# Kernel tuning notes

Hardware: AMD Instinct MI355X
Metric: run time of the kernel (lower is better)

Reference implementation:

```python
import jax, jax.numpy as jnp
import numpy as np

B, N, DIM = 4, 4096, 1024
HEADS, DIM_HEAD, M = 16, 64, 128
DIM_INNER = HEADS * DIM_HEAD
SCALE = DIM_HEAD ** -0.5


def setup_inputs() -> dict:
    key = jax.random.key(0)
    ks = jax.random.split(key, 7)
    x = jax.random.normal(ks[0], (B, N, DIM), dtype=jnp.float32)
    mask = jax.random.bernoulli(ks[1], 0.9, (B, N))  # bool [b, n]
    W_qkv = jax.random.normal(ks[2], (DIM, 3 * DIM_INNER), dtype=jnp.float32) * (DIM ** -0.5)
    agent_tokens = jax.random.normal(ks[3], (HEADS, M, DIM_HEAD), dtype=jnp.float32) * 0.02
    W_qa = jax.random.normal(ks[4], (HEADS, HEADS), dtype=jnp.float32) * (HEADS ** -0.5)
    W_ak = jax.random.normal(ks[5], (HEADS, HEADS), dtype=jnp.float32) * (HEADS ** -0.5)
    W_out = jax.random.normal(ks[6], (DIM_INNER, DIM), dtype=jnp.float32) * (DIM_INNER ** -0.5)
    return {"x": x, "mask": mask, "W_qkv": W_qkv, "agent_tokens": agent_tokens,
            "W_qa": W_qa, "W_ak": W_ak, "W_out": W_out}


def reference(x, mask, W_qkv, agent_tokens, W_qa, W_ak, W_out):
    b, n, _ = x.shape
    h, m, d = agent_tokens.shape
    # qkv projection -> [3, b, h, n, d]  (layout matches 'b n (qkv h d)')
    qkv = (x @ W_qkv).reshape(b, n, 3, h, d).transpose(2, 0, 3, 1, 4)
    q, k, v = qkv[0], qkv[1], qkv[2]
    a = agent_tokens * SCALE  # [h, m, d]
    # stage 1: query-agent similarities [b, h, n, m]
    qa_sim = jnp.einsum('bhid,hjd->bhij', q, a)
    # stage 2: agent-key similarities [b, h, m, n]
    ak_sim = jnp.einsum('hid,bhjd->bhij', a, k)
    max_neg = -jnp.finfo(ak_sim.dtype).max
    ak_sim = jnp.where(mask[:, None, None, :], ak_sim, max_neg)
    qa_attn = jax.nn.softmax(qa_sim, axis=-1)
    ak_attn = jax.nn.softmax(ak_sim, axis=-1)
    # talking heads: 1x1 conv over head dim == head-mixing matmul
    qa_attn = jnp.einsum('gh,bhij->bgij', W_qa, qa_attn)
    ak_attn = jnp.einsum('gh,bhij->bgij', W_ak, ak_attn)
    agent_out = jnp.einsum('bhmn,bhnd->bhmd', ak_attn, v)    # [b, h, m, d]
    out = jnp.einsum('bhnm,bhmd->bhnd', qa_attn, agent_out)  # [b, h, n, d]
    out = jnp.where(mask[:, None, :, None], out, 0.0)
    out = out.transpose(0, 2, 1, 3).reshape(b, n, h * d)
    return out @ W_out
```

## Files before the change

kernel.cpp:

```cpp
#include <hip/hip_runtime.h>
#include <stdint.h>

#define DEVI __device__ __forceinline__

typedef __bf16 bf16x8 __attribute__((ext_vector_type(8)));
typedef float  f32x4  __attribute__((ext_vector_type(4)));
typedef unsigned int u32x2 __attribute__((ext_vector_type(2)));


DEVI unsigned short f2bf(float f) {
  union { float f; unsigned int u; } c; c.f = f;
  return (unsigned short)((c.u + 0x7fffu + ((c.u >> 16) & 1u)) >> 16);
}
DEVI float bf2f(unsigned short s) {
  union { unsigned int u; float f; } c; c.u = ((unsigned int)s) << 16;
  return c.f;
}
DEVI u32x2 pack4(float a, float b, float c, float d) {
  u32x2 r;
  r.x = (unsigned)f2bf(a) | ((unsigned)f2bf(b) << 16);
  r.y = (unsigned)f2bf(c) | ((unsigned)f2bf(d) << 16);
  return r;
}
DEVI bf16x8 ldg8(const unsigned short* p) { return *(const bf16x8*)p; }

DEVI void g2l16(const void* g, void* l) {
  __builtin_amdgcn_global_load_lds(
      (const __attribute__((address_space(1))) unsigned int*)g,
      (__attribute__((address_space(3))) unsigned int*)l, 16, 0, 0);
}

#define MFMA16(acc, a, b) acc = __builtin_amdgcn_mfma_f32_16x16x32_bf16((a), (b), (acc), 0, 0, 0)

#define VMCNT8() asm volatile("s_waitcnt vmcnt(8)")
#define VMCNT4() asm volatile("s_waitcnt vmcnt(4)")
#define VMCNT0() asm volatile("s_waitcnt vmcnt(0)")
#define SBAR()   __builtin_amdgcn_s_barrier()
#define SCHEDB() __builtin_amdgcn_sched_barrier(0)

__global__ __launch_bounds__(256) void k_prep(
    const float* __restrict__ x, const float* __restrict__ Wqkv,
    const float* __restrict__ ag, const float* __restrict__ Wout,
    unsigned short* __restrict__ Xb, unsigned short* __restrict__ WqkvT,
    unsigned short* __restrict__ Ab, unsigned short* __restrict__ WoT,
    float* __restrict__ rowsum)
{
  __shared__ float ldsT[32][33];
  const int tid = threadIdx.x;
  int bx = blockIdx.x;
  if (bx < 16384) {
    size_t i4 = ((size_t)bx * 256 + tid) * 4;
    f32x4 v = *(const f32x4*)&x[i4];
    *(u32x2*)&Xb[i4] = pack4(v[0], v[1], v[2], v[3]);
    return;
  }
  bx -= 16384;
  if (bx < 3072) {
    int jt = bx % 96, kt = bx / 96;
    int r32 = tid >> 3, c4 = (tid & 7) * 4;
    f32x4 v = *(const f32x4*)&Wqkv[(size_t)(kt * 32 + r32) * 3072 + jt * 32 + c4];
#pragma unroll
    for (int i = 0; i < 4; i++) ldsT[r32][c4 + i] = v[i];
    __syncthreads();
    float o0 = ldsT[c4 + 0][r32], o1 = ldsT[c4 + 1][r32];
    float o2 = ldsT[c4 + 2][r32], o3 = ldsT[c4 + 3][r32];
    *(u32x2*)&WqkvT[(size_t)(jt * 32 + r32) * 1024 + kt * 32 + c4] = pack4(o0, o1, o2, o3);
    return;
  }
  bx -= 3072;
  if (bx < 128) {
    size_t i4 = ((size_t)bx * 256 + tid) * 4;
    f32x4 v = *(const f32x4*)&ag[i4];
    *(u32x2*)&Ab[i4] = pack4(v[0] * 0.125f, v[1] * 0.125f, v[2] * 0.125f, v[3] * 0.125f);
    return;
  }
  bx -= 128;
  if (bx < 1024) {
    int ct = bx % 32, dt = bx / 32;
    int r32 = tid >> 3, c4 = (tid & 7) * 4;
    f32x4 v = *(const f32x4*)&Wout[(size_t)(dt * 32 + r32) * 1024 + ct * 32 + c4];
#pragma unroll
    for (int i = 0; i < 4; i++) ldsT[r32][c4 + i] = v[i];
    __syncthreads();
    float o0 = ldsT[c4 + 0][r32], o1 = ldsT[c4 + 1][r32];
    float o2 = ldsT[c4 + 2][r32], o3 = ldsT[c4 + 3][r32];
    *(u32x2*)&WoT[(size_t)(ct * 32 + r32) * 1024 + dt * 32 + c4] = pack4(o0, o1, o2, o3);
    return;
  }
  bx -= 1024;
  {
    const f32x4 z = {0.f, 0.f, 0.f, 0.f};
    *(f32x4*)&rowsum[((size_t)bx * 256 + tid) * 4] = z;
  }
}

DEVI void gemm_core_256(const unsigned short* __restrict__ A,
                        const unsigned short* __restrict__ Bt,
                        int row0, int col0, int swap,
                        unsigned short (*lds)[16384], f32x4 acc[8][4])
{
  const int tid = threadIdx.x, lane = tid & 63, w = tid >> 6;
  const int q = lane >> 4, r = lane & 15;
  const int wm = w >> 2, wn = w & 3;
  const int loff = r * 32 + ((q ^ ((r >> 1) & 3)) << 3);
  const int wslot = w * 512;
  const int scol = ((tid & 3) ^ ((tid >> 3) & 3)) << 3;
  const int srow = tid >> 2;
  const unsigned short* gA0 = A + (size_t)(row0 + srow) * 1024 + scol;
  const unsigned short* gA1 = gA0 + (size_t)128 * 1024;
  const unsigned short* gB0 = Bt + (size_t)(col0 + srow) * 1024 + scol;
  const unsigned short* gB1 = gB0 + (size_t)128 * 1024;
  const int aoff = (swap ? 8192 : 0) + wm * 4096;
  const int boff = (swap ? 0 : 8192) + wn * 2048;

  const f32x4 z = {0.f, 0.f, 0.f, 0.f};
#pragma unroll
  for (int i = 0; i < 8; i++)
#pragma unroll
    for (int j = 0; j < 4; j++) acc[i][j] = z;

#pragma unroll
  for (int pt = 0; pt < 3; ++pt) {
    unsigned short* lr = &lds[pt][0] + wslot;
    g2l16(gA0 + pt * 32, lr);
    g2l16(gA1 + pt * 32, lr + 4096);
    g2l16(gB0 + pt * 32, lr + 8192);
    g2l16(gB1 + pt * 32, lr + 12288);
  }
  VMCNT8();
  SBAR();

  for (int t = 0; t < 32; ++t) {
    const unsigned short* rp = &lds[t & 3][0];
    const unsigned short* pA = rp + aoff + loff;
    const unsigned short* pB = rp + boff + loff;
    bf16x8 af[4], bv[4];
#pragma unroll
    for (int ct = 0; ct < 4; ct++) bv[ct] = *(const bf16x8*)(pB + ct * 512);
#pragma unroll
    for (int rt = 0; rt < 4; rt++) af[rt] = *(const bf16x8*)(pA + rt * 512);
    SCHEDB();
    SBAR();
    if (t < 29) {
      unsigned short* lr = &lds[(t + 3) & 3][0] + wslot;
      size_t ko = (size_t)(t + 3) * 32;
      g2l16(gA0 + ko, lr);
      g2l16(gA1 + ko, lr + 4096);
      g2l16(gB0 + ko, lr + 8192);
      g2l16(gB1 + ko, lr + 12288);
    }
    __builtin_amdgcn_s_setprio(1);
#pragma unroll
    for (int rt = 0; rt < 4; rt++)
#pragma unroll
      for (int ct = 0; ct < 4; ct++) MFMA16(acc[rt][ct], af[rt], bv[ct]);
    __builtin_amdgcn_s_setprio(0);
#pragma unroll
    for (int rt = 0; rt < 4; rt++) af[rt] = *(const bf16x8*)(pA + (rt + 4) * 512);
    SCHEDB();
    if (t < 29)       { VMCNT8(); }
    else if (t == 29) { VMCNT4(); }
    else if (t == 30) { VMCNT0(); }
    SBAR();
    __builtin_amdgcn_s_setprio(1);
#pragma unroll
    for (int rt = 0; rt < 4; rt++)
#pragma unroll
      for (int ct = 0; ct < 4; ct++) MFMA16(acc[rt + 4][ct], af[rt], bv[ct]);
    __builtin_amdgcn_s_setprio(0);
  }
}

__global__ __launch_bounds__(512, 2) void k_gemm_qkv(
    const unsigned short* __restrict__ A, const unsigned short* __restrict__ Bt,
    unsigned short* __restrict__ Q, unsigned short* __restrict__ Kd,
    unsigned short* __restrict__ Vt)
{
  __shared__ __align__(16) unsigned short lds[4][16384];
  const int tid = threadIdx.x, lane = tid & 63, w = tid >> 6;
  const int q = lane >> 4, r = lane & 15, wm = w >> 2, wn = w & 3;
  const int row0 = blockIdx.x * 256, col0 = blockIdx.y * 256;
  const bool qk = blockIdx.y < 8;

  f32x4 acc[8][4];
  gemm_core_256(A, Bt, row0, col0, qk ? 1 : 0, lds, acc);

  const int b = row0 >> 12, row0b = row0 & 4095;
  if (qk) {
    unsigned short* dst = (col0 < 1024) ? Q : Kd;
    const int jb = (col0 & 1023) + wm * 128;
#pragma unroll
    for (int rt = 0; rt < 8; rt++)
#pragma unroll
      for (int ct = 0; ct < 4; ct++) {
        int j = jb + rt * 16 + 4 * q;
        int h = j >> 6, d0 = j & 63;
        int n = row0b + wn * 64 + ct * 16 + r;
        u32x2 pk = pack4(acc[rt][ct][0], acc[rt][ct][1], acc[rt][ct][2], acc[rt][ct][3]);
        *(u32x2*)&dst[(((size_t)(b * 16 + h)) * 4096 + n) * 64 + d0] = pk;
      }
  } else {
    const int jb = (col0 - 2048) + wn * 64;
#pragma unroll
    for (int rt = 0; rt < 8; rt++)
#pragma unroll
      for (int ct = 0; ct < 4; ct++) {
        int j = jb + ct * 16 + r;
        int h = j >> 6, d = j & 63;
        int n = row0b + wm * 128 + rt * 16 + 4 * q;
        u32x2 pk = pack4(acc[rt][ct][0], acc[rt][ct][1], acc[rt][ct][2], acc[rt][ct][3]);
        *(u32x2*)&Vt[(((size_t)(b * 16 + h)) * 64 + d) * 4096 + n] = pk;
      }
  }
}

__global__ __launch_bounds__(256, 2) void k_qk(
    const unsigned short* __restrict__ Q, const unsigned short* __restrict__ Kd,
    const unsigned short* __restrict__ Ab, const int* __restrict__ mask,
    unsigned short* __restrict__ QA, unsigned short* __restrict__ E,
    float* __restrict__ rowsum)
{
  const int tid = threadIdx.x, lane = tid & 63, w = tid >> 6;
  const int q = lane >> 4, r = lane & 15, wr = w >> 1, wc = w & 1;
  const int nt = blockIdx.x, h = blockIdx.y, b = blockIdx.z;
  const unsigned short* Qb = Q + (((size_t)(b * 16 + h)) * 4096 + nt * 128) * 64;
  const unsigned short* Kb = Kd + (((size_t)(b * 16 + h)) * 4096 + nt * 128) * 64;
  const unsigned short* Ah = Ab + (size_t)h * 8192;
  __shared__ float rs[2][128];
  const f32x4 z = {0.f, 0.f, 0.f, 0.f};

  {
    f32x4 acc[4][4];
#pragma unroll
    for (int i = 0; i < 4; i++)
#pragma unroll
      for (int j = 0; j < 4; j++) acc[i][j] = z;
#pragma unroll
    for (int ks = 0; ks < 2; ks++) {
      bf16x8 af[4], bv[4];
#pragma unroll
      for (int rt = 0; rt < 4; rt++) af[rt] = ldg8(Ah + (size_t)(64 * wr + 16 * rt + r) * 64 + ks * 32 + q * 8);
#pragma unroll
      for (int ct = 0; ct < 4; ct++) bv[ct] = ldg8(Qb + (size_t)(64 * wc + 16 * ct + r) * 64 + ks * 32 + q * 8);
#pragma unroll
      for (int rt = 0; rt < 4; rt++)
#pragma unroll
        for (int ct = 0; ct < 4; ct++) MFMA16(acc[rt][ct], af[rt], bv[ct]);
    }
    float cs[4];
#pragma unroll
    for (int ct = 0; ct < 4; ct++) {
      float s = 0.f;
#pragma unroll
      for (int rt = 0; rt < 4; rt++)
#pragma unroll
        for (int reg = 0; reg < 4; reg++) {
          float e = __expf(acc[rt][ct][reg]);
          acc[rt][ct][reg] = e; s += e;
        }
      s += __shfl_xor(s, 16); s += __shfl_xor(s, 32);
      cs[ct] = s;
    }
    if (q == 0) {
#pragma unroll
      for (int ct = 0; ct < 4; ct++) rs[wr][64 * wc + 16 * ct + r] = cs[ct];
    }
    __syncthreads();
#pragma unroll
    for (int ct = 0; ct < 4; ct++) {
      int nl = 64 * wc + 16 * ct + r;
      float inv = 1.0f / (rs[0][nl] + rs[1][nl]);
      int n = nt * 128 + nl;
      size_t base = (((size_t)(b * 16 + h)) * 4096 + n) * 128;
#pragma unroll
      for (int rt = 0; rt < 4; rt++) {
        int m0 = 64 * wr + 16 * rt + 4 * q;
        u32x2 pk = pack4(acc[rt][ct][0] * inv, acc[rt][ct][1] * inv,
                         acc[rt][ct][2] * inv, acc[rt][ct][3] * inv);
        *(u32x2*)&QA[base + m0] = pk;
      }
    }
  }
  __syncthreads();

  {
    f32x4 acc[4][4];
#pragma unroll
    for (int i = 0; i < 4; i++)
#pragma unroll
      for (int j = 0; j < 4; j++) acc[i][j] = z;
#pragma unroll
    for (int ks = 0; ks < 2; ks++) {
      bf16x8 af[4], bv[4];
#pragma unroll
      for (int rt = 0; rt < 4; rt++) af[rt] = ldg8(Kb + (size_t)(64 * wr + 16 * rt + r) * 64 + ks * 32 + q * 8);
#pragma unroll
      for (int ct = 0; ct < 4; ct++) bv[ct] = ldg8(Ah + (size_t)(64 * wc + 16 * ct + r) * 64 + ks * 32 + q * 8);
#pragma unroll
      for (int rt = 0; rt < 4; rt++)
#pragma unroll
        for (int ct = 0; ct < 4; ct++) MFMA16(acc[rt][ct], af[rt], bv[ct]);
    }
    float cs[4] = {0.f, 0.f, 0.f, 0.f};
#pragma unroll
    for (int rt = 0; rt < 4; rt++) {
      const int4 mkv = *(const int4*)&mask[b * 4096 + nt * 128 + 64 * wr + 16 * rt + 4 * q];
      int mka[4] = {mkv.x, mkv.y, mkv.z, mkv.w};
#pragma unroll
      for (int ct = 0; ct < 4; ct++) {
#pragma unroll
        for (int reg = 0; reg < 4; reg++) {
          float e = mka[reg] ? __expf(acc[rt][ct][reg]) : 0.0f;
          acc[rt][ct][reg] = e; cs[ct] += e;
        }
      }
    }
#pragma unroll
    for (int ct = 0; ct < 4; ct++) {
      float s = cs[ct];
      s += __shfl_xor(s, 16); s += __shfl_xor(s, 32);
      cs[ct] = s;
    }
    if (q == 0) {
#pragma unroll
      for (int ct = 0; ct < 4; ct++) rs[wr][64 * wc + 16 * ct + r] = cs[ct];
    }
#pragma unroll
    for (int ct = 0; ct < 4; ct++) {
      int m = 64 * wc + 16 * ct + r;
      size_t base = (((size_t)(b * 16 + h)) * 128 + m) * 4096;
#pragma unroll
      for (int rt = 0; rt < 4; rt++) {
        int n0 = nt * 128 + 64 * wr + 16 * rt + 4 * q;
        u32x2 pk = pack4(acc[rt][ct][0], acc[rt][ct][1], acc[rt][ct][2], acc[rt][ct][3]);
        *(u32x2*)&E[base + n0] = pk;
      }
    }
    __syncthreads();
    if (tid < 128) atomicAdd(&rowsum[(b * 16 + h) * 128 + tid], rs[0][tid] + rs[1][tid]);
  }
}

__global__ __launch_bounds__(256) void k_mix(
    const unsigned short* __restrict__ E, const float* __restrict__ rowsum,
    const float* __restrict__ Wak, unsigned short* __restrict__ MIX)
{
  const int tid = threadIdx.x;
  const int m = blockIdx.y, b = blockIdx.z;
  __shared__ float wv[256];
  __shared__ float inv[16];
  wv[tid] = Wak[tid];
  if (tid < 16) inv[tid] = 1.0f / rowsum[(b * 16 + tid) * 128 + m];
  __syncthreads();
  const int n0 = (blockIdx.x * 256 + tid) * 4;
  float p[16][4];
#pragma unroll
  for (int h = 0; h < 16; h++) {
    u32x2 v = *(const u32x2*)&E[(((size_t)(b * 16 + h)) * 128 + m) * 4096 + n0];
    float iv = inv[h];
    p[h][0] = bf2f((unsigned short)(v.x & 0xffff)) * iv;
    p[h][1] = bf2f((unsigned short)(v.x >> 16)) * iv;
    p[h][2] = bf2f((unsigned short)(v.y & 0xffff)) * iv;
    p[h][3] = bf2f((unsigned short)(v.y >> 16)) * iv;
  }
#pragma unroll
  for (int g = 0; g < 16; g++) {
    float s0 = 0.f, s1 = 0.f, s2 = 0.f, s3 = 0.f;
#pragma unroll
    for (int h = 0; h < 16; h++) {
      float wgh = wv[g * 16 + h];
      s0 += wgh * p[h][0]; s1 += wgh * p[h][1]; s2 += wgh * p[h][2]; s3 += wgh * p[h][3];
    }
    *(u32x2*)&MIX[(((size_t)(b * 16 + g)) * 128 + m) * 4096 + n0] = pack4(s0, s1, s2, s3);
  }
}

__global__ __launch_bounds__(256) void k_ao(
    const unsigned short* __restrict__ MIX, const unsigned short* __restrict__ Vt,
    float* __restrict__ P)
{
  const int tid = threadIdx.x, lane = tid & 63, w4 = tid >> 6;
  const int q = lane >> 4, r = lane & 15;
  const int kc = blockIdx.x, g = blockIdx.y, b = blockIdx.z;
  const unsigned short* Abase = MIX + ((size_t)(b * 16 + g)) * 128 * 4096;
  const unsigned short* Bbase = Vt + ((size_t)(b * 16 + g)) * 64 * 4096;
  f32x4 acc[2][4];
  const f32x4 z = {0.f, 0.f, 0.f, 0.f};
#pragma unroll
  for (int i = 0; i < 2; i++)
#pragma unroll
    for (int j = 0; j < 4; j++) acc[i][j] = z;
  for (int n = kc * 512; n < kc * 512 + 512; n += 32) {
    bf16x8 af[2], bv[4];
#pragma unroll
    for (int rt = 0; rt < 2; rt++) af[rt] = ldg8(Abase + (size_t)(32 * w4 + 16 * rt + r) * 4096 + n + q * 8);
#pragma unroll
    for (int ct = 0; ct < 4; ct++) bv[ct] = ldg8(Bbase + (size_t)(16 * ct + r) * 4096 + n + q * 8);
#pragma unroll
    for (int rt = 0; rt < 2; rt++)
#pragma unroll
      for (int ct = 0; ct < 4; ct++) MFMA16(acc[rt][ct], af[rt], bv[ct]);
  }
  float* Pp = P + (size_t)kc * 524288 + ((size_t)(b * 16 + g)) * 8192;
#pragma unroll
  for (int rt = 0; rt < 2; rt++)
#pragma unroll
    for (int ct = 0; ct < 4; ct++) {
      int m0 = 32 * w4 + 16 * rt + 4 * q, d = 16 * ct + r;
      *(f32x4*)&Pp[(size_t)d * 128 + m0] = acc[rt][ct];
    }
}

__global__ __launch_bounds__(256) void k_aored(
    const float* __restrict__ P, float* __restrict__ AOt)
{
  size_t i = ((size_t)blockIdx.x * 256 + threadIdx.x) * 4;
  f32x4 s = *(const f32x4*)&P[i];
#pragma unroll
  for (int kc = 1; kc < 8; kc++) {
    f32x4 v = *(const f32x4*)&P[(size_t)kc * 524288 + i];
    s[0] += v[0]; s[1] += v[1]; s[2] += v[2]; s[3] += v[3];
  }
  *(f32x4*)&AOt[i] = s;
}

__global__ __launch_bounds__(256) void k_mixqa(
    const unsigned short* __restrict__ QA, const float* __restrict__ Wqa,
    unsigned short* __restrict__ QAmix)
{
  const int tid = threadIdx.x;
  const int b = blockIdx.y;
  __shared__ float wv[256];
  wv[tid] = Wqa[tid];
  __syncthreads();
  const size_t i0 = ((size_t)blockIdx.x * 256 + tid) * 4;
  float p[16][4];
#pragma unroll
  for (int h = 0; h < 16; h++) {
    u32x2 v = *(const u32x2*)&QA[((size_t)(b * 16 + h)) * 524288 + i0];
    p[h][0] = bf2f((unsigned short)(v.x & 0xffff));
    p[h][1] = bf2f((unsigned short)(v.x >> 16));
    p[h][2] = bf2f((unsigned short)(v.y & 0xffff));
    p[h][3] = bf2f((unsigned short)(v.y >> 16));
  }
#pragma unroll
  for (int g = 0; g < 16; g++) {
    float s0 = 0.f, s1 = 0.f, s2 = 0.f, s3 = 0.f;
#pragma unroll
    for (int h = 0; h < 16; h++) {
      float wgh = wv[g * 16 + h];
      s0 += wgh * p[h][0]; s1 += wgh * p[h][1]; s2 += wgh * p[h][2]; s3 += wgh * p[h][3];
    }
    *(u32x2*)&QAmix[((size_t)(b * 16 + g)) * 524288 + i0] = pack4(s0, s1, s2, s3);
  }
}

__global__ __launch_bounds__(256) void k_o1(
    const unsigned short* __restrict__ QAmix, const float* __restrict__ AOt,
    unsigned short* __restrict__ out1)
{
  const int tid = threadIdx.x, lane = tid & 63, w4 = tid >> 6;
  const int q = lane >> 4, r = lane & 15;
  const int nt = blockIdx.x, g = blockIdx.y, b = blockIdx.z;
  const unsigned short* Bbase = QAmix + (((size_t)(b * 16 + g)) * 4096 + nt * 128) * 128;
  const float* Abase = AOt + ((size_t)(b * 16 + g)) * 8192;
  f32x4 acc[4][2];
  const f32x4 z = {0.f, 0.f, 0.f, 0.f};
#pragma unroll
  for (int i = 0; i < 4; i++)
#pragma unroll
    for (int j = 0; j < 2; j++) acc[i][j] = z;
#pragma unroll
  for (int ks = 0; ks < 4; ks++) {
    bf16x8 af[4], bv[2];
#pragma unroll
    for (int rt = 0; rt < 4; rt++) {
      const float* p = Abase + (size_t)(16 * rt + r) * 128 + ks * 32 + q * 8;
      f32x4 f0 = *(const f32x4*)p;
      f32x4 f1 = *(const f32x4*)(p + 4);
      bf16x8 t;
#pragma unroll
      for (int jj = 0; jj < 4; jj++) { t[jj] = (__bf16)f0[jj]; t[4 + jj] = (__bf16)f1[jj]; }
      af[rt] = t;
    }
#pragma unroll
    for (int ct = 0; ct < 2; ct++)
      bv[ct] = ldg8(Bbase + (size_t)(32 * w4 + 16 * ct + r) * 128 + ks * 32 + q * 8);
#pragma unroll
    for (int rt = 0; rt < 4; rt++)
#pragma unroll
      for (int ct = 0; ct < 2; ct++) MFMA16(acc[rt][ct], af[rt], bv[ct]);
  }
#pragma unroll
  for (int ct = 0; ct < 2; ct++) {
    int n = nt * 128 + 32 * w4 + 16 * ct + r;
    size_t base = ((size_t)b * 4096 + n) * 1024 + g * 64;
#pragma unroll
    for (int rt = 0; rt < 4; rt++) {
      int d0 = 16 * rt + 4 * q;
      u32x2 pk = pack4(acc[rt][ct][0], acc[rt][ct][1], acc[rt][ct][2], acc[rt][ct][3]);
      *(u32x2*)&out1[base + d0] = pk;
    }
  }
}

__global__ __launch_bounds__(512, 2) void k_fin2(
    const unsigned short* __restrict__ A, const unsigned short* __restrict__ Bt,
    const int* __restrict__ mask, float* __restrict__ out)
{
  __shared__ __align__(16) unsigned short lds[4][16384];
  const int tid = threadIdx.x, lane = tid & 63, w = tid >> 6;
  const int q = lane >> 4, r = lane & 15, wm = w >> 2, wn = w & 3;
  const int row0 = blockIdx.x * 256, col0 = blockIdx.y * 256;

  f32x4 acc[8][4];
  gemm_core_256(A, Bt, row0, col0, 0, lds, acc);

#pragma unroll
  for (int rt = 0; rt < 8; rt++) {
    const int4 mkv = *(const int4*)&mask[row0 + wm * 128 + rt * 16 + 4 * q];
    int mka[4] = {mkv.x, mkv.y, mkv.z, mkv.w};
#pragma unroll
    for (int reg = 0; reg < 4; reg++) {
      int row = row0 + wm * 128 + rt * 16 + 4 * q + reg;
#pragma unroll
      for (int ct = 0; ct < 4; ct++) {
        int c = col0 + wn * 64 + ct * 16 + r;
        out[(size_t)row * 1024 + c] = mka[reg] ? acc[rt][ct][reg] : 0.0f;
      }
    }
  }
}

extern "C" void kernel_launch(void* const* d_in, const int* in_sizes, int n_in,
                              void* d_out, int out_size, void* d_ws, size_t ws_size,
                              hipStream_t stream) {
  const float* x    = (const float*)d_in[0];
  const int*   mask = (const int*)d_in[1];
  const float* Wqkv = (const float*)d_in[2];
  const float* ag   = (const float*)d_in[3];
  const float* Wqa  = (const float*)d_in[4];
  const float* Wak  = (const float*)d_in[5];
  const float* Wout = (const float*)d_in[6];
  float* out = (float*)d_out;
  char* ws = (char*)d_ws;

  unsigned short* QA    = (unsigned short*)(ws + 0);
  unsigned short* QQ    = (unsigned short*)(ws + 67108864);
  unsigned short* KK    = (unsigned short*)(ws + 67108864 + 33554432);
  unsigned short* MIX   = QQ;
  unsigned short* out1  = QQ;
  unsigned short* VT    = (unsigned short*)(ws + 134217728);
  unsigned short* Xb    = (unsigned short*)(ws + 167772160);
  unsigned short* WqkvT = (unsigned short*)(ws + 167772160 + 33554432);
  unsigned short* E     = Xb;
  float*          Ppart = (float*)Xb;
  unsigned short* QAmix = Xb;
  char* sm = ws + 234881024;
  unsigned short* Ab  = (unsigned short*)(sm);
  unsigned short* WoT = (unsigned short*)(sm + 262144);
  float* rowsum = (float*)(sm + 262144 + 2097152);
  float* AOt    = (float*)(sm + 262144 + 2097152 + 32768);

  k_prep<<<20616, 256, 0, stream>>>(x, Wqkv, ag, Wout, Xb, WqkvT, Ab, WoT, rowsum);
  k_gemm_qkv<<<dim3(64, 12), 512, 0, stream>>>(Xb, WqkvT, QQ, KK, VT);
  k_qk<<<dim3(32, 16, 4), 256, 0, stream>>>(QQ, KK, Ab, mask, QA, E, rowsum);
  k_mix<<<dim3(4, 128, 4), 256, 0, stream>>>(E, rowsum, Wak, MIX);
  k_ao<<<dim3(8, 16, 4), 256, 0, stream>>>(MIX, VT, Ppart);
  k_aored<<<512, 256, 0, stream>>>(Ppart, AOt);
  k_mixqa<<<dim3(512, 4), 256, 0, stream>>>(QA, Wqa, QAmix);
  k_o1<<<dim3(32, 16, 4), 256, 0, stream>>>(QAmix, AOt, out1);
  k_fin2<<<dim3(64, 4), 512, 0, stream>>>(out1, WoT, mask, out);
}
```

Baseline: 462.5 us.

## Rework shared GEMM core to 4 waves with 128x128 warp tiles and BK=64 double buffering

The 256x256 GEMM core used by the QKV projection and output projection now runs with 4 waves instead of 8. Each wave computes a 128x128 sub-tile (8x8 MFMA accumulators), and the K loop uses a 64-wide step with a two-stage LDS double buffer in place of a four-stage 32-wide ring. The aim is to raise register-level reuse per LDS fragment load and to halve the number of barriers per K step. In exchange it uses 256 accumulator VGPRs per lane at occupancy 1, waits on vmcnt(0) every iteration, and drops the setprio and sched_barrier interleaving, so latency hiding may suffer.

Measured after the change: 579.4 us. 1.25x slower.

```diff
diff --git a/kernel.cpp b/kernel.cpp
--- a/kernel.cpp
+++ b/kernel.cpp
@@ -32,11 +32,8 @@
 
 #define MFMA16(acc, a, b) acc = __builtin_amdgcn_mfma_f32_16x16x32_bf16((a), (b), (acc), 0, 0, 0)
 
-#define VMCNT8() asm volatile("s_waitcnt vmcnt(8)")
-#define VMCNT4() asm volatile("s_waitcnt vmcnt(4)")
 #define VMCNT0() asm volatile("s_waitcnt vmcnt(0)")
 #define SBAR()   __builtin_amdgcn_s_barrier()
-#define SCHEDB() __builtin_amdgcn_sched_barrier(0)
 
 __global__ __launch_bounds__(256) void k_prep(
     const float* __restrict__ x, const float* __restrict__ Wqkv,
@@ -97,92 +94,83 @@
 DEVI void gemm_core_256(const unsigned short* __restrict__ A,
                         const unsigned short* __restrict__ Bt,
                         int row0, int col0, int swap,
-                        unsigned short (*lds)[16384], f32x4 acc[8][4])
+                        unsigned short* ldsS, f32x4 acc[8][8])
 {
   const int tid = threadIdx.x, lane = tid & 63, w = tid >> 6;
   const int q = lane >> 4, r = lane & 15;
-  const int wm = w >> 2, wn = w & 3;
-  const int loff = r * 32 + ((q ^ ((r >> 1) & 3)) << 3);
-  const int wslot = w * 512;
-  const int scol = ((tid & 3) ^ ((tid >> 3) & 3)) << 3;
-  const int srow = tid >> 2;
-  const unsigned short* gA0 = A + (size_t)(row0 + srow) * 1024 + scol;
-  const unsigned short* gA1 = gA0 + (size_t)128 * 1024;
-  const unsigned short* gB0 = Bt + (size_t)(col0 + srow) * 1024 + scol;
-  const unsigned short* gB1 = gB0 + (size_t)128 * 1024;
-  const int aoff = (swap ? 8192 : 0) + wm * 4096;
-  const int boff = (swap ? 0 : 8192) + wn * 2048;
+  const int wm = w >> 1, wn = w & 1;
+  const int gr = tid >> 3;
+  const int scol = ((tid & 7) ^ ((tid >> 3) & 7)) << 3;
+  const unsigned short* gA = A + (size_t)(row0 + gr) * 1024 + scol;
+  const unsigned short* gB = Bt + (size_t)(col0 + gr) * 1024 + scol;
+  const int ldst = w * 512;
+  const int aoff = (swap ? 16384 : 0) + wm * 8192;
+  const int boff = (swap ? 0 : 16384) + wn * 8192;
+  const int cs0 = (q ^ (r & 7)) << 3;
+  const int cs1 = ((q + 4) ^ (r & 7)) << 3;
+  const int rb = r * 64;
 
   const f32x4 z = {0.f, 0.f, 0.f, 0.f};
 #pragma unroll
   for (int i = 0; i < 8; i++)
 #pragma unroll
-    for (int j = 0; j < 4; j++) acc[i][j] = z;
-
-#pragma unroll
-  for (int pt = 0; pt < 3; ++pt) {
-    unsigned short* lr = &lds[pt][0] + wslot;
-    g2l16(gA0 + pt * 32, lr);
-    g2l16(gA1 + pt * 32, lr + 4096);
-    g2l16(gB0 + pt * 32, lr + 8192);
-    g2l16(gB1 + pt * 32, lr + 12288);
-  }
-  VMCNT8();
+    for (int j = 0; j < 8; j++) acc[i][j] = z;
+
+  auto stage = [&](int p, int ks) {
+    unsigned short* dA = ldsS + p * 32768 + ldst;
+    unsigned short* dB = dA + 16384;
+    const unsigned short* sA = gA + ks * 64;
+    const unsigned short* sB = gB + ks * 64;
+#pragma unroll
+    for (int j = 0; j < 8; ++j) {
+      g2l16(sA + (size_t)j * 32768, dA + j * 2048);
+      g2l16(sB + (size_t)j * 32768, dB + j * 2048);
+    }
+  };
+
+  stage(0, 0);
+  VMCNT0();
   SBAR();
 
-  for (int t = 0; t < 32; ++t) {
-    const unsigned short* rp = &lds[t & 3][0];
-    const unsigned short* pA = rp + aoff + loff;
-    const unsigned short* pB = rp + boff + loff;
-    bf16x8 af[4], bv[4];
-#pragma unroll
-    for (int ct = 0; ct < 4; ct++) bv[ct] = *(const bf16x8*)(pB + ct * 512);
-#pragma unroll
-    for (int rt = 0; rt < 4; rt++) af[rt] = *(const bf16x8*)(pA + rt * 512);
-    SCHEDB();
+  for (int t = 0; t < 16; ++t) {
+    const int p = t & 1;
+    if (t < 15) stage(p ^ 1, t + 1);
+    const unsigned short* bufA = ldsS + p * 32768 + aoff;
+    const unsigned short* bufB = ldsS + p * 32768 + boff;
+    bf16x8 af[8], bv[8];
+#pragma unroll
+    for (int i = 0; i < 8; ++i) af[i] = *(const bf16x8*)&bufA[rb + i * 1024 + cs0];
+#pragma unroll
+    for (int i = 0; i < 8; ++i) bv[i] = *(const bf16x8*)&bufB[rb + i * 1024 + cs0];
+#pragma unroll
+    for (int rt = 0; rt < 8; ++rt)
+#pragma unroll
+      for (int ct = 0; ct < 8; ++ct) MFMA16(acc[rt][ct], af[rt], bv[ct]);
+#pragma unroll
+    for (int i = 0; i < 8; ++i) af[i] = *(const bf16x8*)&bufA[rb + i * 1024 + cs1];
+#pragma unroll
+    for (int i = 0; i < 8; ++i) bv[i] = *(const bf16x8*)&bufB[rb + i * 1024 + cs1];
+#pragma unroll
+    for (int rt = 0; rt < 8; ++rt)
+#pragma unroll
+      for (int ct = 0; ct < 8; ++ct) MFMA16(acc[rt][ct], af[rt], bv[ct]);
+    VMCNT0();
     SBAR();
-    if (t < 29) {
-      unsigned short* lr = &lds[(t + 3) & 3][0] + wslot;
-      size_t ko = (size_t)(t + 3) * 32;
-      g2l16(gA0 + ko, lr);
-      g2l16(gA1 + ko, lr + 4096);
-      g2l16(gB0 + ko, lr + 8192);
-      g2l16(gB1 + ko, lr + 12288);
-    }
-    __builtin_amdgcn_s_setprio(1);
-#pragma unroll
-    for (int rt = 0; rt < 4; rt++)
-#pragma unroll
-      for (int ct = 0; ct < 4; ct++) MFMA16(acc[rt][ct], af[rt], bv[ct]);
-    __builtin_amdgcn_s_setprio(0);
-#pragma unroll
-    for (int rt = 0; rt < 4; rt++) af[rt] = *(const bf16x8*)(pA + (rt + 4) * 512);
-    SCHEDB();
-    if (t < 29)       { VMCNT8(); }
-    else if (t == 29) { VMCNT4(); }
-    else if (t == 30) { VMCNT0(); }
-    SBAR();
-    __builtin_amdgcn_s_setprio(1);
-#pragma unroll
-    for (int rt = 0; rt < 4; rt++)
-#pragma unroll
-      for (int ct = 0; ct < 4; ct++) MFMA16(acc[rt + 4][ct], af[rt], bv[ct]);
-    __builtin_amdgcn_s_setprio(0);
-  }
-}
-
-__global__ __launch_bounds__(512, 2) void k_gemm_qkv(
+  }
+}
+
+__global__ __launch_bounds__(256, 1) void k_gemm_qkv(
     const unsigned short* __restrict__ A, const unsigned short* __restrict__ Bt,
     unsigned short* __restrict__ Q, unsigned short* __restrict__ Kd,
     unsigned short* __restrict__ Vt)
 {
-  __shared__ __align__(16) unsigned short lds[4][16384];
+  __shared__ __align__(16) unsigned short lds[65536];
   const int tid = threadIdx.x, lane = tid & 63, w = tid >> 6;
-  const int q = lane >> 4, r = lane & 15, wm = w >> 2, wn = w & 3;
+  const int q = lane >> 4, r = lane & 15, wm = w >> 1, wn = w & 1;
   const int row0 = blockIdx.x * 256, col0 = blockIdx.y * 256;
   const bool qk = blockIdx.y < 8;
 
-  f32x4 acc[8][4];
+  f32x4 acc[8][8];
   gemm_core_256(A, Bt, row0, col0, qk ? 1 : 0, lds, acc);
 
   const int b = row0 >> 12, row0b = row0 & 4095;
@@ -192,19 +180,19 @@
 #pragma unroll
     for (int rt = 0; rt < 8; rt++)
 #pragma unroll
-      for (int ct = 0; ct < 4; ct++) {
+      for (int ct = 0; ct < 8; ct++) {
         int j = jb + rt * 16 + 4 * q;
         int h = j >> 6, d0 = j & 63;
-        int n = row0b + wn * 64 + ct * 16 + r;
+        int n = row0b + wn * 128 + ct * 16 + r;
         u32x2 pk = pack4(acc[rt][ct][0], acc[rt][ct][1], acc[rt][ct][2], acc[rt][ct][3]);
         *(u32x2*)&dst[(((size_t)(b * 16 + h)) * 4096 + n) * 64 + d0] = pk;
       }
   } else {
-    const int jb = (col0 - 2048) + wn * 64;
+    const int jb = (col0 - 2048) + wn * 128;
 #pragma unroll
     for (int rt = 0; rt < 8; rt++)
 #pragma unroll
-      for (int ct = 0; ct < 4; ct++) {
+      for (int ct = 0; ct < 8; ct++) {
         int j = jb + ct * 16 + r;
         int h = j >> 6, d = j & 63;
         int n = row0b + wm * 128 + rt * 16 + 4 * q;
@@ -504,16 +492,16 @@
   }
 }
 
-__global__ __launch_bounds__(512, 2) void k_fin2(
+__global__ __launch_bounds__(256, 1) void k_fin2(
     const unsigned short* __restrict__ A, const unsigned short* __restrict__ Bt,
     const int* __restrict__ mask, float* __restrict__ out)
 {
-  __shared__ __align__(16) unsigned short lds[4][16384];
+  __shared__ __align__(16) unsigned short lds[65536];
   const int tid = threadIdx.x, lane = tid & 63, w = tid >> 6;
-  const int q = lane >> 4, r = lane & 15, wm = w >> 2, wn = w & 3;
+  const int q = lane >> 4, r = lane & 15, wm = w >> 1, wn = w & 1;
   const int row0 = blockIdx.x * 256, col0 = blockIdx.y * 256;
 
-  f32x4 acc[8][4];
+  f32x4 acc[8][8];
   gemm_core_256(A, Bt, row0, col0, 0, lds, acc);
 
 #pragma unroll
@@ -524,8 +512,8 @@
     for (int reg = 0; reg < 4; reg++) {
       int row = row0 + wm * 128 + rt * 16 + 4 * q + reg;
 #pragma unroll
-      for (int ct = 0; ct < 4; ct++) {
-        int c = col0 + wn * 64 + ct * 16 + r;
+      for (int ct = 0; ct < 8; ct++) {
+        int c = col0 + wn * 128 + ct * 16 + r;
         out[(size_t)row * 1024 + c] = mka[reg] ? acc[rt][ct][reg] : 0.0f;
       }
     }
@@ -563,12 +551,12 @@
   float* AOt    = (float*)(sm + 262144 + 2097152 + 32768);
 
   k_prep<<<20616, 256, 0, stream>>>(x, Wqkv, ag, Wout, Xb, WqkvT, Ab, WoT, rowsum);
-  k_gemm_qkv<<<dim3(64, 12), 512, 0, stream>>>(Xb, WqkvT, QQ, KK, VT);
+  k_gemm_qkv<<<dim3(64, 12), 256, 0, stream>>>(Xb, WqkvT, QQ, KK, VT);
   k_qk<<<dim3(32, 16, 4), 256, 0, stream>>>(QQ, KK, Ab, mask, QA, E, rowsum);
   k_mix<<<dim3(4, 128, 4), 256, 0, stream>>>(E, rowsum, Wak, MIX);
   k_ao<<<dim3(8, 16, 4), 256, 0, stream>>>(MIX, VT, Ppart);
   k_aored<<<512, 256, 0, stream>>>(Ppart, AOt);
   k_mixqa<<<dim3(512, 4), 256, 0, stream>>>(QA, Wqa, QAmix);
   k_o1<<<dim3(32, 16, 4), 256, 0, stream>>>(QAmix, AOt, out1);
-  k_fin2<<<dim3(64, 4), 512, 0, stream>>>(out1, WoT, mask, out);
-}
+  k_fin2<<<dim3(64, 4), 256, 0, stream>>>(out1, WoT, mask, out);
+}
```
